# Kernel optimization log

Measured on AMD Instinct MI355X. Metric: run time of the kernel, lower is better.

## Reference

```python
import jax, jax.numpy as jnp
import numpy as np

N, E, D, H, L = 20000, 320000, 128, 8, 3
C = D // H  # per-head channels = 16


def setup_inputs() -> dict:
    key = jax.random.key(0)
    ks = jax.random.split(key, 20)
    s = 1.0 / np.sqrt(D)
    inp = {
        "x": jax.random.normal(ks[0], (N, D), dtype=jnp.float32),
        "edge_index": jax.random.randint(ks[1], (2, E), 0, N, dtype=jnp.int64),
        "Wq": jax.random.normal(ks[2], (L, D, D), dtype=jnp.float32) * s,
        "bq": jnp.zeros((L, D), dtype=jnp.float32),
        "Wk": jax.random.normal(ks[3], (L, D, D), dtype=jnp.float32) * s,
        "bk": jnp.zeros((L, D), dtype=jnp.float32),
        "Wv": jax.random.normal(ks[4], (L, D, D), dtype=jnp.float32) * s,
        "bv": jnp.zeros((L, D), dtype=jnp.float32),
        "Wskip": jax.random.normal(ks[5], (L, D, D), dtype=jnp.float32) * s,
        "bskip": jnp.zeros((L, D), dtype=jnp.float32),
        "Wbeta": jax.random.normal(ks[6], (L, 3 * D, 1), dtype=jnp.float32) * (1.0 / np.sqrt(3 * D)),
        "ln_g": jnp.ones((L, D), dtype=jnp.float32),
        "ln_b": jnp.zeros((L, D), dtype=jnp.float32),
        "Wout": jax.random.normal(ks[7], (D, D), dtype=jnp.float32) * s,
        "bout": jnp.zeros((D,), dtype=jnp.float32),
    }
    return inp


def _layer_norm(x, g, b, eps=1e-5):
    mu = jnp.mean(x, axis=-1, keepdims=True)
    var = jnp.mean(jnp.square(x - mu), axis=-1, keepdims=True)
    return (x - mu) * jax.lax.rsqrt(var + eps) * g + b


def _transformer_conv(x, src, dst, Wq, bq, Wk, bk, Wv, bv, Wskip, bskip, Wbeta):
    # project q/k/v: [N, D] -> [N, H, C]
    q = (x @ Wq + bq).reshape(N, H, C)
    k = (x @ Wk + bk).reshape(N, H, C)
    v = (x @ Wv + bv).reshape(N, H, C)
    # per-edge attention logits: [E, H]
    alpha = jnp.sum(q[dst] * k[src], axis=-1) / np.sqrt(C)
    # scatter-softmax over edges grouped by dst node
    m = jax.ops.segment_max(alpha, dst, num_segments=N)  # [N, H]
    m = jnp.where(jnp.isfinite(m), m, 0.0)
    ea = jnp.exp(alpha - m[dst])
    denom = jax.ops.segment_sum(ea, dst, num_segments=N)  # [N, H]
    attn = ea / (denom[dst] + 1e-16)  # [E, H]
    # weighted message aggregation: [N, H, C] -> [N, D]
    out = jax.ops.segment_sum(attn[:, :, None] * v[src], dst, num_segments=N)
    out = out.reshape(N, D)
    # beta-gated skip connection (beta=True, root_weight=True)
    x_r = x @ Wskip + bskip
    beta = jax.nn.sigmoid(jnp.concatenate([out, x_r, out - x_r], axis=-1) @ Wbeta)  # [N, 1]
    return beta * x_r + (1.0 - beta) * out


def reference(x, edge_index, Wq, bq, Wk, bk, Wv, bv, Wskip, bskip, Wbeta, ln_g, ln_b, Wout, bout):
    src, dst = edge_index[0], edge_index[1]
    for i in range(L):
        residual = x
        x = _transformer_conv(x, src, dst, Wq[i], bq[i], Wk[i], bk[i], Wv[i], bv[i],
                              Wskip[i], bskip[i], Wbeta[i])
        x = jax.nn.relu(x)  # dropout is identity in eval mode
        x = _layer_norm(x + residual, ln_g[i], ln_b[i])
    return x @ Wout + bout
```

## Files before the change

kernel.cpp:

```cpp
#include <hip/hip_runtime.h>

#define N_NODES 20000
#define N_EDGES 320000
#define DIM 128
#define NLAYER 3
#define SCAN_BLK 1024
#define N_SCAN_BLKS ((N_NODES + SCAN_BLK - 1) / SCAN_BLK)
#define LDS_STRIDE 136

#define PREP_CASTW_BLKS 208
#define PREP_ZERO_BLKS 79
#define PREP_TOTAL (PREP_CASTW_BLKS + PREP_ZERO_BLKS)

typedef __attribute__((ext_vector_type(8))) short short8;
typedef __attribute__((ext_vector_type(4))) float f32x4;
typedef __attribute__((ext_vector_type(2))) float f32x2;

__device__ inline ushort f2bf(float f) {
  uint u = __float_as_uint(f);
  uint r = (u + 0x7fffu + ((u >> 16) & 1u)) >> 16;
  return (ushort)r;
}
__device__ inline float bf2f(ushort u) { return __uint_as_float(((uint)u) << 16); }

__device__ inline uint f2fp8(float f) {
  return __builtin_amdgcn_cvt_pk_fp8_f32(f, 0.f, 0, false) & 0xffu;
}
__device__ inline void fp8x4_to_f32(uint w, float* o) {
  f32x2 lo = __builtin_amdgcn_cvt_pk_f32_fp8(w, false);
  f32x2 hi = __builtin_amdgcn_cvt_pk_f32_fp8(w, true);
  o[0] = lo[0]; o[1] = lo[1]; o[2] = hi[0]; o[3] = hi[1];
}

__global__ __launch_bounds__(256) void prep_kernel(
    const float* __restrict__ Wq, const float* __restrict__ Wk,
    const float* __restrict__ Wv, const float* __restrict__ Ws,
    const float* __restrict__ Wo, ushort* __restrict__ wt,
    int* __restrict__ degc, int* __restrict__ bsum) {
  int b = blockIdx.x;
  int t = threadIdx.x;
  if (b < PREP_CASTW_BLKS) {
    int z = b >> 4;
    int r = b & 15;
    int k0 = (r >> 2) * 32, n0 = (r & 3) * 32;
    const float* src;
    if (z < 12) {
      int l = z >> 2, j = z & 3;
      src = (j == 0 ? Wq : j == 1 ? Wk : j == 2 ? Wv : Ws) + (size_t)l * DIM * DIM;
    } else {
      src = Wo;
    }
    __shared__ float tile[32][33];
    int tx = t & 31, ty = t >> 5;
    #pragma unroll
    for (int i = 0; i < 32; i += 8)
      tile[ty + i][tx] = src[(size_t)(k0 + ty + i) * DIM + n0 + tx];
    __syncthreads();
    ushort* dst = wt + (size_t)z * DIM * DIM;
    #pragma unroll
    for (int i = 0; i < 32; i += 8)
      dst[(size_t)(n0 + ty + i) * DIM + k0 + tx] = f2bf(tile[tx][ty + i]);
  } else {
    int i = (b - PREP_CASTW_BLKS) * 256 + t;
    if (i < N_NODES) degc[i] = 0;
    else if (i < N_NODES + N_SCAN_BLKS) bsum[i - N_NODES] = 0;
  }
}


__global__ void count_deg_kernel(const int* __restrict__ ei, int* __restrict__ deg) {
  int e = blockIdx.x * 256 + threadIdx.x;
  if (e < N_EDGES) atomicAdd(&deg[ei[N_EDGES + e]], 1);
}

__global__ __launch_bounds__(SCAN_BLK) void scan_lookback_kernel(
    int* __restrict__ degc, int* __restrict__ rowptr, int* __restrict__ bsum) {
  __shared__ int wsum[16];
  __shared__ int prevs;
  int t = threadIdx.x, lane = t & 63, w = t >> 6, bid = blockIdx.x;
  int i = bid * SCAN_BLK + t;
  int val = (i < N_NODES) ? degc[i] : 0;
  if (i < N_NODES) degc[i] = 0;
  int s = val;
  #pragma unroll
  for (int off = 1; off < 64; off <<= 1) {
    int u = __shfl_up(s, off);
    if (lane >= off) s += u;
  }
  if (lane == 63) wsum[w] = s;
  __syncthreads();
  if (t < 16) {
    int wv = wsum[t];
    int ss = wv;
    #pragma unroll
    for (int off = 1; off < 16; off <<= 1) {
      int u = __shfl_up(ss, off);
      if (t >= off) ss += u;
    }
    wsum[t] = ss - wv;
  }
  __syncthreads();
  int excl = wsum[w] + s - val;
  if (t == SCAN_BLK - 1)
    __hip_atomic_store(&bsum[bid], excl + val + 1, __ATOMIC_RELEASE,
                       __HIP_MEMORY_SCOPE_AGENT);
  if (w == 0) {
    int p = 0;
    for (int j = lane; j < bid; j += 64) {
      int v;
      do {
        v = __hip_atomic_load(&bsum[j], __ATOMIC_ACQUIRE, __HIP_MEMORY_SCOPE_AGENT);
      } while (v == 0);
      p += v - 1;
    }
    #pragma unroll
    for (int off = 1; off < 64; off <<= 1) p += __shfl_xor(p, off);
    if (t == 0) prevs = p;
  }
  __syncthreads();
  int off0 = prevs;
  if (i < N_NODES) rowptr[i] = off0 + excl;
  if (bid == N_SCAN_BLKS - 1 && t == SCAN_BLK - 1) rowptr[N_NODES] = off0 + excl + val;
}

__global__ void scatter_kernel(const int* __restrict__ ei, const int* __restrict__ rowptr,
                               int* __restrict__ cursor, int* __restrict__ csr_src) {
  int e = blockIdx.x * 256 + threadIdx.x;
  if (e < N_EDGES) {
    int d = ei[N_EDGES + e];
    int s = ei[e];
    int pos = atomicAdd(&cursor[d], 1);
    csr_src[rowptr[d] + pos] = s;
  }
}

template <int IN_F32>
__global__ __launch_bounds__(256) void gemm_mfma_kernel(
    const void* __restrict__ Xp, const ushort* __restrict__ WT,
    const float* __restrict__ B0, const float* __restrict__ B1,
    const float* __restrict__ B2, const float* __restrict__ B3,
    void* __restrict__ O0, void* __restrict__ O1, void* __restrict__ O2,
    void* __restrict__ O3, int m0, int m1, int m2, int m3) {
  __shared__ ushort As[128 * LDS_STRIDE];
  int mat = blockIdx.y;
  const ushort* Wt = WT + (size_t)mat * DIM * DIM;
  const float* bias;
  void* O;
  int mode;
  switch (mat) {
    case 0: bias = B0; O = O0; mode = m0; break;
    case 1: bias = B1; O = O1; mode = m1; break;
    case 2: bias = B2; O = O2; mode = m2; break;
    default: bias = B3; O = O3; mode = m3; break;
  }
  int t = threadIdx.x;
  int wid = t >> 6, lane = t & 63;
  int row0 = blockIdx.x * 128;
  int wr = wid >> 1, wc = wid & 1;
  int lr = lane & 15;
  int kc8 = (lane >> 4) * 8;

  if (IN_F32) {
    const float* Xf = (const float*)Xp;
    int rowi = t >> 5;
    int col4 = (t & 31) * 4;
    #pragma unroll
    for (int pass = 0; pass < 16; ++pass) {
      int row = pass * 8 + rowi;
      int gr = min(row0 + row, N_NODES - 1);
      float4 f = *(const float4*)(Xf + (size_t)gr * DIM + col4);
      ushort4 u;
      u.x = f2bf(f.x); u.y = f2bf(f.y); u.z = f2bf(f.z); u.w = f2bf(f.w);
      *(ushort4*)(As + row * LDS_STRIDE + col4) = u;
    }
  } else {
    const ushort* X = (const ushort*)Xp;
    int rowi = t >> 4;
    int col = (t & 15) * 8;
    #pragma unroll
    for (int pass = 0; pass < 8; ++pass) {
      int row = pass * 16 + rowi;
      int gr = min(row0 + row, N_NODES - 1);
      short8 val = *(const short8*)(X + (size_t)gr * DIM + col);
      *(short8*)(As + row * LDS_STRIDE + col) = val;
    }
  }
  __syncthreads();

  f32x4 acc[4][4];
  #pragma unroll
  for (int i = 0; i < 4; ++i)
    #pragma unroll
    for (int j = 0; j < 4; ++j) acc[i][j] = (f32x4){0.f, 0.f, 0.f, 0.f};

  #pragma unroll
  for (int ks = 0; ks < 4; ++ks) {
    short8 b[4];
    #pragma unroll
    for (int cf = 0; cf < 4; ++cf) {
      int c = wc * 64 + cf * 16 + lr;
      b[cf] = *(const short8*)(Wt + (size_t)c * DIM + ks * 32 + kc8);
    }
    #pragma unroll
    for (int rf = 0; rf < 4; ++rf) {
      int r = wr * 64 + rf * 16 + lr;
      short8 a = *(const short8*)(As + r * LDS_STRIDE + ks * 32 + kc8);
      #pragma unroll
      for (int cf = 0; cf < 4; ++cf)
        acc[rf][cf] = __builtin_amdgcn_mfma_f32_16x16x32_bf16(a, b[cf], acc[rf][cf], 0, 0, 0);
    }
  }

  #pragma unroll
  for (int cf = 0; cf < 4; ++cf) {
    int c = wc * 64 + cf * 16 + lr;
    float bv = bias[c];
    #pragma unroll
    for (int rf = 0; rf < 4; ++rf) {
      #pragma unroll
      for (int reg = 0; reg < 4; ++reg) {
        int r = row0 + wr * 64 + rf * 16 + (lane >> 4) * 4 + reg;
        if (r < N_NODES) {
          float val = acc[rf][cf][reg] + bv;
          if (mode == 0)
            ((ushort*)O)[(size_t)r * DIM + c] = f2bf(val);
          else if (mode == 1)
            ((float*)O)[(size_t)r * DIM + c] = val;
          else if (mode == 2)
            ((unsigned char*)O)[(size_t)r * 256 + c] = (unsigned char)f2fp8(val);
          else
            ((unsigned char*)O)[(size_t)r * 256 + 128 + c] = (unsigned char)f2fp8(val);
        }
      }
    }
  }
}

template <int RES_F32>
__global__ __launch_bounds__(256) void attn_fused_kernel(
    const ushort* __restrict__ q, const unsigned char* __restrict__ kv,
    const ushort* __restrict__ xr, const void* __restrict__ xres,
    const int* __restrict__ rowptr, const int* __restrict__ csr_src,
    const float* __restrict__ wbeta, const float* __restrict__ lng,
    const float* __restrict__ lnb, ushort* __restrict__ xnextb) {
  __shared__ float red[4][8][8][20];
  int w = threadIdx.x >> 6;
  int lane = threadIdx.x & 63;
  int n = blockIdx.x * 4 + w;
  int h = lane & 7, e = lane >> 3;

  const ushort* qrow = q + (size_t)n * DIM + h * 16;
  short8 q0 = *(const short8*)qrow;
  short8 q1 = *(const short8*)(qrow + 8);
  float qf[16];
  #pragma unroll
  for (int i = 0; i < 8; ++i) {
    qf[i] = bf2f((ushort)q0[i]) * 0.25f;
    qf[8 + i] = bf2f((ushort)q1[i]) * 0.25f;
  }

  int s0 = rowptr[n];
  int deg = rowptr[n + 1] - s0;
  float acc[16];
  #pragma unroll
  for (int i = 0; i < 16; ++i) acc[i] = 0.f;
  float dsum = 0.f;

  int src_n = (deg > 0) ? csr_src[s0 + min(e, deg - 1)] : 0;
  for (int base = 0; base < deg; base += 8) {
    int idx = base + e;
    bool valid = idx < deg;
    int src = src_n;
    if (base + 8 < deg)
      src_n = csr_src[s0 + min(base + 8 + e, deg - 1)];
    const unsigned char* rec = kv + (size_t)src * 256 + h * 16;
    uint4 ku = *(const uint4*)rec;
    uint4 vu = *(const uint4*)(rec + 128);
    float kf[16], vf[16];
    fp8x4_to_f32(ku.x, kf + 0);
    fp8x4_to_f32(ku.y, kf + 4);
    fp8x4_to_f32(ku.z, kf + 8);
    fp8x4_to_f32(ku.w, kf + 12);
    fp8x4_to_f32(vu.x, vf + 0);
    fp8x4_to_f32(vu.y, vf + 4);
    fp8x4_to_f32(vu.z, vf + 8);
    fp8x4_to_f32(vu.w, vf + 12);
    float p = 0.f;
    #pragma unroll
    for (int i = 0; i < 16; ++i) p = fmaf(qf[i], kf[i], p);
    float ea = __expf(p);
    ea = valid ? ea : 0.f;
    dsum += ea;
    #pragma unroll
    for (int i = 0; i < 16; ++i) acc[i] = fmaf(ea, vf[i], acc[i]);
  }

  {
    float* my = &red[w][e][h][0];
    *(float4*)(my + 0) = make_float4(acc[0], acc[1], acc[2], acc[3]);
    *(float4*)(my + 4) = make_float4(acc[4], acc[5], acc[6], acc[7]);
    *(float4*)(my + 8) = make_float4(acc[8], acc[9], acc[10], acc[11]);
    *(float4*)(my + 12) = make_float4(acc[12], acc[13], acc[14], acc[15]);
    my[16] = dsum;
  }
  asm volatile("s_waitcnt lgkmcnt(0)" ::: "memory");

  int c0 = lane * 2;
  int hh = lane >> 3, cc = (lane & 7) * 2;
  float o0 = 0.f, o1 = 0.f, den = 0.f;
  #pragma unroll
  for (int ee = 0; ee < 8; ++ee) {
    float2 tv = *(float2*)&red[w][ee][hh][cc];
    o0 += tv.x;
    o1 += tv.y;
    den += red[w][ee][hh][16];
  }
  float inv = 1.f / (den + 1e-16f);
  o0 *= inv;
  o1 *= inv;

  ushort2 xru = *(const ushort2*)(xr + (size_t)n * DIM + c0);
  float xr0 = bf2f(xru.x), xr1 = bf2f(xru.y);
  float wa0 = wbeta[c0] + wbeta[2 * DIM + c0];
  float wa1 = wbeta[c0 + 1] + wbeta[2 * DIM + c0 + 1];
  float wb0 = wbeta[DIM + c0] - wbeta[2 * DIM + c0];
  float wb1 = wbeta[DIM + c0 + 1] - wbeta[2 * DIM + c0 + 1];
  float bs = o0 * wa0 + o1 * wa1 + xr0 * wb0 + xr1 * wb1;
  #pragma unroll
  for (int off = 1; off < 64; off <<= 1) bs += __shfl_xor(bs, off);
  float beta = 1.f / (1.f + __expf(-bs));
  float y0 = fmaxf(beta * xr0 + (1.f - beta) * o0, 0.f);
  float y1 = fmaxf(beta * xr1 + (1.f - beta) * o1, 0.f);
  float rv0, rv1;
  if (RES_F32) {
    float2 rv = *(const float2*)((const float*)xres + (size_t)n * DIM + c0);
    rv0 = rv.x; rv1 = rv.y;
  } else {
    ushort2 ru = *(const ushort2*)((const ushort*)xres + (size_t)n * DIM + c0);
    rv0 = bf2f(ru.x); rv1 = bf2f(ru.y);
  }
  y0 += rv0;
  y1 += rv1;
  float s = y0 + y1;
  #pragma unroll
  for (int off = 1; off < 64; off <<= 1) s += __shfl_xor(s, off);
  float mu = s * (1.f / 128.f);
  float d0 = y0 - mu, d1 = y1 - mu;
  float vs = d0 * d0 + d1 * d1;
  #pragma unroll
  for (int off = 1; off < 64; off <<= 1) vs += __shfl_xor(vs, off);
  float rstd = rsqrtf(vs * (1.f / 128.f) + 1e-5f);
  float2 g = *(const float2*)(lng + c0);
  float2 b = *(const float2*)(lnb + c0);
  float out0 = d0 * rstd * g.x + b.x;
  float out1 = d1 * rstd * g.y + b.y;
  ushort2 ob;
  ob.x = f2bf(out0);
  ob.y = f2bf(out1);
  *(ushort2*)(xnextb + (size_t)n * DIM + c0) = ob;
}


extern "C" void kernel_launch(void* const* d_in, const int* in_sizes, int n_in,
                              void* d_out, int out_size, void* d_ws, size_t ws_size,
                              hipStream_t stream) {
  const float* x_in = (const float*)d_in[0];
  const int* ei = (const int*)d_in[1];
  const float* Wq = (const float*)d_in[2];
  const float* bq = (const float*)d_in[3];
  const float* Wk = (const float*)d_in[4];
  const float* bk = (const float*)d_in[5];
  const float* Wv = (const float*)d_in[6];
  const float* bv = (const float*)d_in[7];
  const float* Wsk = (const float*)d_in[8];
  const float* bsk = (const float*)d_in[9];
  const float* Wb = (const float*)d_in[10];
  const float* lng = (const float*)d_in[11];
  const float* lnb = (const float*)d_in[12];
  const float* Wout = (const float*)d_in[13];
  const float* bout = (const float*)d_in[14];
  float* out = (float*)d_out;

  char* p = (char*)d_ws;
  auto alloc = [&](size_t bytes) {
    char* r = p;
    p += (bytes + 255) & ~(size_t)255;
    return r;
  };
  const size_t NB2 = (size_t)N_NODES * DIM * 2;
  ushort* xbb = (ushort*)alloc(NB2);
  ushort* qb = (ushort*)alloc(NB2);
  unsigned char* kvb = (unsigned char*)alloc((size_t)N_NODES * 256);
  ushort* xrb = (ushort*)alloc(NB2);
  ushort* wt = (ushort*)alloc((size_t)13 * DIM * DIM * 2);
  int* rowptr = (int*)alloc((N_NODES + 1) * 4);
  int* degc = (int*)alloc(N_NODES * 4);
  int* bsum = (int*)alloc(N_SCAN_BLKS * 4);
  int* csr_src = (int*)alloc(N_EDGES * 4);

  prep_kernel<<<PREP_TOTAL, 256, 0, stream>>>(Wq, Wk, Wv, Wsk, Wout, wt, degc, bsum);
  count_deg_kernel<<<(N_EDGES + 255) / 256, 256, 0, stream>>>(ei, degc);
  scan_lookback_kernel<<<N_SCAN_BLKS, SCAN_BLK, 0, stream>>>(degc, rowptr, bsum);
  scatter_kernel<<<(N_EDGES + 255) / 256, 256, 0, stream>>>(ei, rowptr, degc, csr_src);

  const int GX = (N_NODES + 127) / 128;
  for (int l = 0; l < NLAYER; ++l) {
    if (l == 0) {
      gemm_mfma_kernel<1><<<dim3(GX, 4), 256, 0, stream>>>(
          (const void*)x_in, wt + (size_t)l * 4 * DIM * DIM,
          bq + (size_t)l * DIM, bk + (size_t)l * DIM, bv + (size_t)l * DIM,
          bsk + (size_t)l * DIM,
          qb, kvb, kvb, xrb, 0, 2, 3, 0);
      attn_fused_kernel<1><<<N_NODES / 4, 256, 0, stream>>>(
          qb, kvb, xrb, (const void*)x_in, rowptr, csr_src,
          Wb + (size_t)l * 3 * DIM, lng + (size_t)l * DIM, lnb + (size_t)l * DIM,
          xbb);
    } else {
      gemm_mfma_kernel<0><<<dim3(GX, 4), 256, 0, stream>>>(
          (const void*)xbb, wt + (size_t)l * 4 * DIM * DIM,
          bq + (size_t)l * DIM, bk + (size_t)l * DIM, bv + (size_t)l * DIM,
          bsk + (size_t)l * DIM,
          qb, kvb, kvb, xrb, 0, 2, 3, 0);
      attn_fused_kernel<0><<<N_NODES / 4, 256, 0, stream>>>(
          qb, kvb, xrb, (const void*)xbb, rowptr, csr_src,
          Wb + (size_t)l * 3 * DIM, lng + (size_t)l * DIM, lnb + (size_t)l * DIM,
          xbb);
    }
  }
  gemm_mfma_kernel<0><<<dim3(GX, 1), 256, 0, stream>>>(
      (const void*)xbb, wt + (size_t)12 * DIM * DIM, bout, bout, bout, bout,
      out, out, out, out, 1, 1, 1, 1);
}
```

Measured before the change: 193.0 us.

## Remap attention lanes to two heads per lane and sixteen edges per wave iteration

Each lane of the fused attention kernel now handles 32 channels (two heads) of 16 edges per iteration instead of one head of 8 edges. This halves the number of loop iterations per node and issues wider K/V loads per lane. The partial sums are first combined with cross-lane shuffles before a smaller LDS reduction. In exchange, register use roughly doubles (32 accumulators plus 32 q values) and many shuffles are added, which may lower occupancy. The wider per-edge load pattern can also waste lanes on low-degree nodes.

```diff
diff --git a/kernel.cpp b/kernel.cpp
--- a/kernel.cpp
+++ b/kernel.cpp
@@ -243,77 +243,100 @@
     const int* __restrict__ rowptr, const int* __restrict__ csr_src,
     const float* __restrict__ wbeta, const float* __restrict__ lng,
     const float* __restrict__ lnb, ushort* __restrict__ xnextb) {
-  __shared__ float red[4][8][8][20];
+  __shared__ float red[4][4][4][36];
   int w = threadIdx.x >> 6;
   int lane = threadIdx.x & 63;
   int n = blockIdx.x * 4 + w;
-  int h = lane & 7, e = lane >> 3;
-
-  const ushort* qrow = q + (size_t)n * DIM + h * 16;
-  short8 q0 = *(const short8*)qrow;
-  short8 q1 = *(const short8*)(qrow + 8);
-  float qf[16];
-  #pragma unroll
-  for (int i = 0; i < 8; ++i) {
-    qf[i] = bf2f((ushort)q0[i]) * 0.25f;
-    qf[8 + i] = bf2f((ushort)q1[i]) * 0.25f;
+  int s = lane & 3, e = lane >> 2;
+
+  const ushort* qrow = q + (size_t)n * DIM + s * 32;
+  float qf[32];
+  #pragma unroll
+  for (int j = 0; j < 4; ++j) {
+    short8 qv = *(const short8*)(qrow + j * 8);
+    #pragma unroll
+    for (int i = 0; i < 8; ++i) qf[j * 8 + i] = bf2f((ushort)qv[i]) * 0.25f;
   }
 
   int s0 = rowptr[n];
   int deg = rowptr[n + 1] - s0;
-  float acc[16];
-  #pragma unroll
-  for (int i = 0; i < 16; ++i) acc[i] = 0.f;
-  float dsum = 0.f;
+  float acc[32];
+  #pragma unroll
+  for (int i = 0; i < 32; ++i) acc[i] = 0.f;
+  float dsumA = 0.f, dsumB = 0.f;
 
   int src_n = (deg > 0) ? csr_src[s0 + min(e, deg - 1)] : 0;
-  for (int base = 0; base < deg; base += 8) {
+  for (int base = 0; base < deg; base += 16) {
     int idx = base + e;
     bool valid = idx < deg;
     int src = src_n;
-    if (base + 8 < deg)
-      src_n = csr_src[s0 + min(base + 8 + e, deg - 1)];
-    const unsigned char* rec = kv + (size_t)src * 256 + h * 16;
-    uint4 ku = *(const uint4*)rec;
-    uint4 vu = *(const uint4*)(rec + 128);
-    float kf[16], vf[16];
-    fp8x4_to_f32(ku.x, kf + 0);
-    fp8x4_to_f32(ku.y, kf + 4);
-    fp8x4_to_f32(ku.z, kf + 8);
-    fp8x4_to_f32(ku.w, kf + 12);
-    fp8x4_to_f32(vu.x, vf + 0);
-    fp8x4_to_f32(vu.y, vf + 4);
-    fp8x4_to_f32(vu.z, vf + 8);
-    fp8x4_to_f32(vu.w, vf + 12);
-    float p = 0.f;
-    #pragma unroll
-    for (int i = 0; i < 16; ++i) p = fmaf(qf[i], kf[i], p);
-    float ea = __expf(p);
-    ea = valid ? ea : 0.f;
-    dsum += ea;
-    #pragma unroll
-    for (int i = 0; i < 16; ++i) acc[i] = fmaf(ea, vf[i], acc[i]);
-  }
-
-  {
-    float* my = &red[w][e][h][0];
-    *(float4*)(my + 0) = make_float4(acc[0], acc[1], acc[2], acc[3]);
-    *(float4*)(my + 4) = make_float4(acc[4], acc[5], acc[6], acc[7]);
-    *(float4*)(my + 8) = make_float4(acc[8], acc[9], acc[10], acc[11]);
-    *(float4*)(my + 12) = make_float4(acc[12], acc[13], acc[14], acc[15]);
-    my[16] = dsum;
+    if (base + 16 < deg)
+      src_n = csr_src[s0 + min(base + 16 + e, deg - 1)];
+    const unsigned char* rec = kv + (size_t)src * 256 + s * 32;
+    uint4 ku0 = *(const uint4*)rec;
+    uint4 ku1 = *(const uint4*)(rec + 16);
+    uint4 vu0 = *(const uint4*)(rec + 128);
+    uint4 vu1 = *(const uint4*)(rec + 144);
+    float tf[32];
+    fp8x4_to_f32(ku0.x, tf + 0);
+    fp8x4_to_f32(ku0.y, tf + 4);
+    fp8x4_to_f32(ku0.z, tf + 8);
+    fp8x4_to_f32(ku0.w, tf + 12);
+    fp8x4_to_f32(ku1.x, tf + 16);
+    fp8x4_to_f32(ku1.y, tf + 20);
+    fp8x4_to_f32(ku1.z, tf + 24);
+    fp8x4_to_f32(ku1.w, tf + 28);
+    float pA = 0.f, pB = 0.f;
+    #pragma unroll
+    for (int i = 0; i < 16; ++i) pA = fmaf(qf[i], tf[i], pA);
+    #pragma unroll
+    for (int i = 16; i < 32; ++i) pB = fmaf(qf[i], tf[i], pB);
+    float eaA = valid ? __expf(pA) : 0.f;
+    float eaB = valid ? __expf(pB) : 0.f;
+    dsumA += eaA;
+    dsumB += eaB;
+    fp8x4_to_f32(vu0.x, tf + 0);
+    fp8x4_to_f32(vu0.y, tf + 4);
+    fp8x4_to_f32(vu0.z, tf + 8);
+    fp8x4_to_f32(vu0.w, tf + 12);
+    fp8x4_to_f32(vu1.x, tf + 16);
+    fp8x4_to_f32(vu1.y, tf + 20);
+    fp8x4_to_f32(vu1.z, tf + 24);
+    fp8x4_to_f32(vu1.w, tf + 28);
+    #pragma unroll
+    for (int i = 0; i < 16; ++i) acc[i] = fmaf(eaA, tf[i], acc[i]);
+    #pragma unroll
+    for (int i = 16; i < 32; ++i) acc[i] = fmaf(eaB, tf[i], acc[i]);
+  }
+
+  #pragma unroll
+  for (int off = 4; off <= 8; off <<= 1) {
+    dsumA += __shfl_xor(dsumA, off);
+    dsumB += __shfl_xor(dsumB, off);
+    #pragma unroll
+    for (int i = 0; i < 32; ++i) acc[i] += __shfl_xor(acc[i], off);
+  }
+  if ((e & 3) == 0) {
+    float* my = &red[w][e >> 2][s][0];
+    #pragma unroll
+    for (int i = 0; i < 32; i += 4)
+      *(float4*)(my + i) = make_float4(acc[i], acc[i + 1], acc[i + 2], acc[i + 3]);
+    my[32] = dsumA;
+    my[33] = dsumB;
   }
   asm volatile("s_waitcnt lgkmcnt(0)" ::: "memory");
 
   int c0 = lane * 2;
-  int hh = lane >> 3, cc = (lane & 7) * 2;
+  int sp = lane >> 4;
+  int ci = c0 & 31;
+  int hbit = (ci >> 4) & 1;
   float o0 = 0.f, o1 = 0.f, den = 0.f;
   #pragma unroll
-  for (int ee = 0; ee < 8; ++ee) {
-    float2 tv = *(float2*)&red[w][ee][hh][cc];
+  for (int g = 0; g < 4; ++g) {
+    float2 tv = *(float2*)&red[w][g][sp][ci];
     o0 += tv.x;
     o1 += tv.y;
-    den += red[w][ee][hh][16];
+    den += red[w][g][sp][32 + hbit];
   }
   float inv = 1.f / (den + 1e-16f);
   o0 *= inv;
@@ -341,10 +364,10 @@
   }
   y0 += rv0;
   y1 += rv1;
-  float s = y0 + y1;
-  #pragma unroll
-  for (int off = 1; off < 64; off <<= 1) s += __shfl_xor(s, off);
-  float mu = s * (1.f / 128.f);
+  float sm = y0 + y1;
+  #pragma unroll
+  for (int off = 1; off < 64; off <<= 1) sm += __shfl_xor(sm, off);
+  float mu = sm * (1.f / 128.f);
   float d0 = y0 - mu, d1 = y1 - mu;
   float vs = d0 * d0 + d1 * d1;
   #pragma unroll
```

After: 221.9 us. 15.0% more time.
